# Kernel optimization log

Measured on AMD Instinct MI355X. Metric: run time of the kernel, lower is better.

The kernel has to match this reference:

```python
import jax, jax.numpy as jnp
import numpy as np

EPS = 1e-6
P = 0.8
NUM_CLASSES = 1604
BATCH = 16384


def _make_seesaw_matrix(key, num_classes, p):
    # Synthetic long-tailed class counts standing in for the CSV bincount.
    counts = jax.random.randint(key, (num_classes,), 1, 10000).astype(jnp.float32)
    cond = counts[:, None] > counts[None, :]
    ratio = (counts[None, :] / counts[:, None]) ** p
    return jnp.where(cond, ratio, jnp.ones_like(ratio))  # [C, C]


def setup_inputs() -> dict:
    key = jax.random.key(0)
    k_log, k_tgt, k_cnt = jax.random.split(key, 3)
    logits = jax.random.normal(k_log, (BATCH, NUM_CLASSES), dtype=jnp.float32)
    targets = jax.random.randint(k_tgt, (BATCH,), 0, NUM_CLASSES)
    s = _make_seesaw_matrix(k_cnt, NUM_CLASSES, P)
    return {"logits": logits, "s": s, "targets": targets}


def reference(logits, s, targets):
    # logits: [B, C], s: [C, C], targets: [B] int
    C = s.shape[0]
    onehot = jax.nn.one_hot(targets, C, dtype=logits.dtype)  # [B, C]
    logits = logits - jnp.max(logits, axis=-1, keepdims=True)
    numerator = jnp.exp(logits)  # [B, C]
    # denom[b, i] = sum_j (1 - t[b, j]) * s[i, j] * exp(logits[b, j]) + exp(logits[b, i])
    # Expressed as a GEMM instead of the original [B, C, C] broadcast.
    denominator = jnp.einsum('bj,ij->bi', (1.0 - onehot) * numerator, s) + numerator
    sigma = numerator / (denominator + EPS)
    loss = -(onehot * jnp.log(sigma + EPS)).sum(axis=-1)  # [B]
    return loss.mean()
```

## Files before the change

kernel.cpp:

```cpp
#include <hip/hip_runtime.h>
#include <math.h>

#define EPS 1e-6f
#define C 1604
#define B 16384
#define C4 401
#define BLOCK 256

__global__ __launch_bounds__(BLOCK) void seesaw_row_kernel(
    const float* __restrict__ logits,
    const float* __restrict__ s,
    const int*   __restrict__ targets,
    float*       __restrict__ block_loss)
{
    const int b    = blockIdx.x;
    const int tid  = threadIdx.x;
    const int wave = tid >> 6;
    const int lane = tid & 63;
    const int t    = targets[b];

    const float4* lrow = (const float4*)(logits + (size_t)b * C);
    const float4* srow = (const float4*)(s + (size_t)t * C);

    const bool has1 = (tid + BLOCK) < C4;

    float4 v0 = lrow[tid];
    float4 v1 = has1 ? lrow[tid + BLOCK]
                     : make_float4(-INFINITY, -INFINITY, -INFINITY, -INFINITY);

    float m = fmaxf(fmaxf(v0.x, v0.y), fmaxf(v0.z, v0.w));
    m = fmaxf(m, fmaxf(fmaxf(v1.x, v1.y), fmaxf(v1.z, v1.w)));

    #pragma unroll
    for (int off = 32; off > 0; off >>= 1)
        m = fmaxf(m, __shfl_down(m, off, 64));

    __shared__ float swav[4];
    __shared__ float s_m;
    __shared__ float s_numt;
    if (lane == 0) swav[wave] = m;
    __syncthreads();
    if (tid == 0)
        s_m = fmaxf(fmaxf(swav[0], swav[1]), fmaxf(swav[2], swav[3]));
    __syncthreads();
    m = s_m;

    const int t4 = t >> 2;
    if (t4 == tid || (has1 && t4 == tid + BLOCK)) {
        float4 v = (t4 == tid) ? v0 : v1;
        int r = t & 3;
        float lt = (r == 0) ? v.x : (r == 1) ? v.y : (r == 2) ? v.z : v.w;
        s_numt = __expf(lt - m);
    }

    float4 sr0 = srow[tid];
    float4 sr1 = has1 ? srow[tid + BLOCK] : make_float4(0.f, 0.f, 0.f, 0.f);

    float partial = 0.f;
    {
        int j = tid << 2;
        partial += __expf(v0.x - m) * ((j    ) == t ? 1.0f : sr0.x);
        partial += __expf(v0.y - m) * ((j + 1) == t ? 1.0f : sr0.y);
        partial += __expf(v0.z - m) * ((j + 2) == t ? 1.0f : sr0.z);
        partial += __expf(v0.w - m) * ((j + 3) == t ? 1.0f : sr0.w);
    }
    if (has1) {
        int j = (tid + BLOCK) << 2;
        partial += __expf(v1.x - m) * ((j    ) == t ? 1.0f : sr1.x);
        partial += __expf(v1.y - m) * ((j + 1) == t ? 1.0f : sr1.y);
        partial += __expf(v1.z - m) * ((j + 2) == t ? 1.0f : sr1.z);
        partial += __expf(v1.w - m) * ((j + 3) == t ? 1.0f : sr1.w);
    }

    #pragma unroll
    for (int off = 32; off > 0; off >>= 1)
        partial += __shfl_down(partial, off, 64);
    if (lane == 0) swav[wave] = partial;
    __syncthreads();

    if (tid == 0) {
        float denom = (swav[0] + swav[1]) + (swav[2] + swav[3]);
        float sigma = s_numt / (denom + EPS);
        block_loss[b] = -logf(sigma + EPS);
    }
}

__global__ __launch_bounds__(BLOCK) void seesaw_reduce_kernel(
    const float* __restrict__ in, float* __restrict__ out)
{
    const int tid = threadIdx.x;
    const float4* in4 = (const float4*)in;
    float acc = 0.f;
    #pragma unroll
    for (int i = tid; i < B / 4; i += BLOCK) {
        float4 v = in4[i];
        acc += (v.x + v.y) + (v.z + v.w);
    }
    #pragma unroll
    for (int off = 32; off > 0; off >>= 1)
        acc += __shfl_down(acc, off, 64);
    __shared__ float sw[4];
    if ((tid & 63) == 0) sw[tid >> 6] = acc;
    __syncthreads();
    if (tid == 0)
        out[0] = ((sw[0] + sw[1]) + (sw[2] + sw[3])) * (1.0f / B);
}

extern "C" void kernel_launch(void* const* d_in, const int* in_sizes, int n_in,
                              void* d_out, int out_size, void* d_ws, size_t ws_size,
                              hipStream_t stream) {
    const float* logits  = (const float*)d_in[0];
    const float* s       = (const float*)d_in[1];
    const int*   targets = (const int*)d_in[2];
    float* out        = (float*)d_out;
    float* block_loss = (float*)d_ws;

    seesaw_row_kernel<<<B, BLOCK, 0, stream>>>(logits, s, targets, block_loss);
    seesaw_reduce_kernel<<<1, BLOCK, 0, stream>>>(block_loss, out);
}
```

Before: 166.5 us.

## Map one wavefront per row to drop block-level syncs and shared memory

Each 64-lane wave now handles a whole row, and each block covers four rows. Every lane holds seven float4 chunks of logits and of the seesaw row in registers, so the max and sum reductions use only wave shuffles with no __syncthreads or LDS. The target logit is fetched with a shuffle instead of shared memory. The final reduction kernel grows to 1024 threads. This raises per-thread register use and gives each wave more serial memory work in exchange for removing block barriers.

```diff
diff --git a/kernel.cpp b/kernel.cpp
--- a/kernel.cpp
+++ b/kernel.cpp
@@ -6,104 +6,95 @@
 #define B 16384
 #define C4 401
 #define BLOCK 256
+#define ROWS_PER_BLOCK 4
+#define TAIL_LANES (C4 - 6 * 64)
 
 __global__ __launch_bounds__(BLOCK) void seesaw_row_kernel(
     const float* __restrict__ logits,
     const float* __restrict__ s,
     const int*   __restrict__ targets,
-    float*       __restrict__ block_loss)
+    float*       __restrict__ row_loss)
 {
-    const int b    = blockIdx.x;
-    const int tid  = threadIdx.x;
-    const int wave = tid >> 6;
-    const int lane = tid & 63;
-    const int t    = targets[b];
+    const int wave = threadIdx.x >> 6;
+    const int lane = threadIdx.x & 63;
+    const int b = blockIdx.x * ROWS_PER_BLOCK + wave;
+    const int t = targets[b];
 
     const float4* lrow = (const float4*)(logits + (size_t)b * C);
     const float4* srow = (const float4*)(s + (size_t)t * C);
 
-    const bool has1 = (tid + BLOCK) < C4;
+    float4 lv[7], sv[7];
+    #pragma unroll
+    for (int k = 0; k < 6; ++k) lv[k] = lrow[lane + 64 * k];
+    #pragma unroll
+    for (int k = 0; k < 6; ++k) sv[k] = srow[lane + 64 * k];
+    const bool tail = lane < TAIL_LANES;
+    lv[6] = tail ? lrow[lane + 384]
+                 : make_float4(-INFINITY, -INFINITY, -INFINITY, -INFINITY);
+    sv[6] = tail ? srow[lane + 384] : make_float4(0.f, 0.f, 0.f, 0.f);
 
-    float4 v0 = lrow[tid];
-    float4 v1 = has1 ? lrow[tid + BLOCK]
-                     : make_float4(-INFINITY, -INFINITY, -INFINITY, -INFINITY);
-
-    float m = fmaxf(fmaxf(v0.x, v0.y), fmaxf(v0.z, v0.w));
-    m = fmaxf(m, fmaxf(fmaxf(v1.x, v1.y), fmaxf(v1.z, v1.w)));
-
+    float m = -INFINITY;
+    #pragma unroll
+    for (int k = 0; k < 7; ++k)
+        m = fmaxf(m, fmaxf(fmaxf(lv[k].x, lv[k].y), fmaxf(lv[k].z, lv[k].w)));
     #pragma unroll
     for (int off = 32; off > 0; off >>= 1)
-        m = fmaxf(m, __shfl_down(m, off, 64));
+        m = fmaxf(m, __shfl_xor(m, off, 64));
 
-    __shared__ float swav[4];
-    __shared__ float s_m;
-    __shared__ float s_numt;
-    if (lane == 0) swav[wave] = m;
-    __syncthreads();
-    if (tid == 0)
-        s_m = fmaxf(fmaxf(swav[0], swav[1]), fmaxf(swav[2], swav[3]));
-    __syncthreads();
-    m = s_m;
-
-    const int t4 = t >> 2;
-    if (t4 == tid || (has1 && t4 == tid + BLOCK)) {
-        float4 v = (t4 == tid) ? v0 : v1;
-        int r = t & 3;
-        float lt = (r == 0) ? v.x : (r == 1) ? v.y : (r == 2) ? v.z : v.w;
-        s_numt = __expf(lt - m);
+    float p = 0.f;
+    float lt_local = 0.f;
+    #pragma unroll
+    for (int k = 0; k < 7; ++k) {
+        const int j = (lane + 64 * k) << 2;
+        const bool e0 = (j     == t);
+        const bool e1 = (j + 1 == t);
+        const bool e2 = (j + 2 == t);
+        const bool e3 = (j + 3 == t);
+        p += __expf(lv[k].x - m) * (e0 ? 1.f : sv[k].x);
+        p += __expf(lv[k].y - m) * (e1 ? 1.f : sv[k].y);
+        p += __expf(lv[k].z - m) * (e2 ? 1.f : sv[k].z);
+        p += __expf(lv[k].w - m) * (e3 ? 1.f : sv[k].w);
+        if (e0) lt_local = lv[k].x;
+        if (e1) lt_local = lv[k].y;
+        if (e2) lt_local = lv[k].z;
+        if (e3) lt_local = lv[k].w;
     }
-
-    float4 sr0 = srow[tid];
-    float4 sr1 = has1 ? srow[tid + BLOCK] : make_float4(0.f, 0.f, 0.f, 0.f);
-
-    float partial = 0.f;
-    {
-        int j = tid << 2;
-        partial += __expf(v0.x - m) * ((j    ) == t ? 1.0f : sr0.x);
-        partial += __expf(v0.y - m) * ((j + 1) == t ? 1.0f : sr0.y);
-        partial += __expf(v0.z - m) * ((j + 2) == t ? 1.0f : sr0.z);
-        partial += __expf(v0.w - m) * ((j + 3) == t ? 1.0f : sr0.w);
-    }
-    if (has1) {
-        int j = (tid + BLOCK) << 2;
-        partial += __expf(v1.x - m) * ((j    ) == t ? 1.0f : sr1.x);
-        partial += __expf(v1.y - m) * ((j + 1) == t ? 1.0f : sr1.y);
-        partial += __expf(v1.z - m) * ((j + 2) == t ? 1.0f : sr1.z);
-        partial += __expf(v1.w - m) * ((j + 3) == t ? 1.0f : sr1.w);
-    }
-
     #pragma unroll
     for (int off = 32; off > 0; off >>= 1)
-        partial += __shfl_down(partial, off, 64);
-    if (lane == 0) swav[wave] = partial;
-    __syncthreads();
+        p += __shfl_xor(p, off, 64);
 
-    if (tid == 0) {
-        float denom = (swav[0] + swav[1]) + (swav[2] + swav[3]);
-        float sigma = s_numt / (denom + EPS);
-        block_loss[b] = -logf(sigma + EPS);
+    const float lt = __shfl(lt_local, (t >> 2) & 63, 64);
+
+    if (lane == 0) {
+        const float numt  = __expf(lt - m);
+        const float sigma = numt / (p + EPS);
+        row_loss[b] = -logf(sigma + EPS);
     }
 }
 
-__global__ __launch_bounds__(BLOCK) void seesaw_reduce_kernel(
+__global__ __launch_bounds__(1024) void seesaw_reduce_kernel(
     const float* __restrict__ in, float* __restrict__ out)
 {
     const int tid = threadIdx.x;
     const float4* in4 = (const float4*)in;
     float acc = 0.f;
     #pragma unroll
-    for (int i = tid; i < B / 4; i += BLOCK) {
+    for (int i = tid; i < B / 4; i += 1024) {
         float4 v = in4[i];
         acc += (v.x + v.y) + (v.z + v.w);
     }
     #pragma unroll
     for (int off = 32; off > 0; off >>= 1)
-        acc += __shfl_down(acc, off, 64);
-    __shared__ float sw[4];
+        acc += __shfl_xor(acc, off, 64);
+    __shared__ float sw[16];
     if ((tid & 63) == 0) sw[tid >> 6] = acc;
     __syncthreads();
-    if (tid == 0)
-        out[0] = ((sw[0] + sw[1]) + (sw[2] + sw[3])) * (1.0f / B);
+    if (tid == 0) {
+        float s0 = 0.f;
+        #pragma unroll
+        for (int w = 0; w < 16; ++w) s0 += sw[w];
+        out[0] = s0 * (1.0f / B);
+    }
 }
 
 extern "C" void kernel_launch(void* const* d_in, const int* in_sizes, int n_in,
@@ -112,9 +103,9 @@
     const float* logits  = (const float*)d_in[0];
     const float* s       = (const float*)d_in[1];
     const int*   targets = (const int*)d_in[2];
-    float* out        = (float*)d_out;
-    float* block_loss = (float*)d_ws;
+    float* out      = (float*)d_out;
+    float* row_loss = (float*)d_ws;
 
-    seesaw_row_kernel<<<B, BLOCK, 0, stream>>>(logits, s, targets, block_loss);
-    seesaw_reduce_kernel<<<1, BLOCK, 0, stream>>>(block_loss, out);
+    seesaw_row_kernel<<<B / ROWS_PER_BLOCK, BLOCK, 0, stream>>>(logits, s, targets, row_loss);
+    seesaw_reduce_kernel<<<1, 1024, 0, stream>>>(row_loss, out);
 }
```

Result: no change. 163.9 us (-1.6%).
